# Kernel optimization log

Measured on AMD Instinct MI355X. Metric: run time of the kernel, lower is better.

## Reference

```python
import jax, jax.numpy as jnp
import numpy as np

BATCH, T, S, M = 512, 4096, 64, 125  # batch, seq_len, n_states, emission alphabet (5^3)


def setup_inputs() -> dict:
    key = jax.random.key(0)
    k1, k2, k3, k4 = jax.random.split(key, 4)
    obs = jax.random.randint(k1, (BATCH, T), 0, M)
    x = jax.nn.one_hot(obs, M, dtype=jnp.float32)            # [B, T, M] one-hot emissions
    I = jax.nn.softmax(jax.random.normal(k2, (1, S)))        # initial state distribution [1, S]
    A = jax.nn.softmax(jax.random.normal(k3, (S, S)), axis=-1)   # transition matrix, rows sum to 1
    Bm = jax.nn.softmax(jax.random.normal(k4, (M, S)), axis=0)   # emission matrix, cols sum to 1
    return {"x": x, "I": I, "A": A, "Bm": Bm}


def reference(x, I, A, Bm):
    """HMM forward algorithm with per-step normalization (default scaling branch of CgpHmmCell).

    Returns the accumulated log-likelihood [B, 1].
    """
    xT = jnp.swapaxes(x, 0, 1)  # [T, B, M] for scan over time

    # t = 1: R = I (broadcast over batch), old_loglik = 0
    E0 = xT[0] @ Bm                                  # [B, S]
    u0 = E0 * I                                      # unscaled alpha
    Z0 = jnp.sum(u0, axis=1, keepdims=True)          # [B, 1]
    carry0 = (u0 / Z0, jnp.log(Z0))

    def step(carry, x_t):
        alpha, ll = carry
        R = alpha @ A                                # [B, S] transition
        E = x_t @ Bm                                 # [B, S] emission lookup (one-hot matmul)
        u = E * R
        Z = jnp.sum(u, axis=1, keepdims=True)        # per-sequence scaling factor
        return (u / Z, ll + jnp.log(Z)), None

    (alpha, loglik), _ = jax.lax.scan(step, carry0, xT[1:])
    return loglik
```

## Files before the change

kernel.cpp:

```cpp
#include <hip/hip_runtime.h>


#define BATCH 512
#define T 4096
#define S 64
#define M 125
#define NPACK 22
#define WPB 4
#define BSTR 68
#define WSTR 17

typedef __attribute__((ext_vector_type(8))) short bf16x8;
typedef __attribute__((ext_vector_type(4))) float f32x4;

union BFU { unsigned u[4]; bf16x8 v; };

__device__ __forceinline__ unsigned pk_bf16(float a, float b) {
    unsigned ua = __float_as_uint(a) + 0x8000u;
    unsigned ub = __float_as_uint(b) + 0x8000u;
    return (ub & 0xFFFF0000u) | (ua >> 16);
}
__device__ __forceinline__ unsigned pk_bf16_rne(float a, float b) {
    unsigned ua = __float_as_uint(a); ua += 0x7FFFu + ((ua >> 16) & 1u);
    unsigned ub = __float_as_uint(b); ub += 0x7FFFu + ((ub >> 16) & 1u);
    return (ub & 0xFFFF0000u) | (ua >> 16);
}

__global__ __launch_bounds__(256) void extract_obs(const float4* __restrict__ x4,
                                                   unsigned char* __restrict__ obs) {
    const long long n4 = (long long)BATCH * T * M / 4;
    long long stride = (long long)gridDim.x * blockDim.x;
    for (long long i = (long long)blockIdx.x * blockDim.x + threadIdx.x; i < n4; i += stride) {
        float4 v = x4[i];
        if (v.x != 0.0f || v.y != 0.0f || v.z != 0.0f || v.w != 0.0f) {
            long long e = i * 4;
            if (v.x != 0.0f) { long long r = (e + 0) / M; obs[r] = (unsigned char)(e + 0 - r * M); }
            if (v.y != 0.0f) { long long r = (e + 1) / M; obs[r] = (unsigned char)(e + 1 - r * M); }
            if (v.z != 0.0f) { long long r = (e + 2) / M; obs[r] = (unsigned char)(e + 2 - r * M); }
            if (v.w != 0.0f) { long long r = (e + 3) / M; obs[r] = (unsigned char)(e + 3 - r * M); }
        }
    }
}

__global__ __launch_bounds__(256) void hmm_mfma(const unsigned char* __restrict__ obs,
                                                const float* __restrict__ Iv,
                                                const float* __restrict__ A,
                                                const float* __restrict__ Bm,
                                                float* __restrict__ out) {
    __shared__ __align__(16) float BmL[M * BSTR];
    __shared__ __align__(16) float ILds[S];
    __shared__ unsigned wscAll[WPB][32 * WSTR];

    const int tid = threadIdx.x, wv = tid >> 6, lane = tid & 63;
    const int s = lane & 15, g = lane >> 4;

    for (int i = tid; i < M * S; i += 256) BmL[(i >> 6) * BSTR + (i & 63)] = Bm[i];
    if (tid < S) ILds[tid] = Iv[tid];
    __syncthreads();

    BFU Af[4][2];
#pragma unroll
    for (int mt = 0; mt < 4; ++mt)
#pragma unroll
        for (int kf = 0; kf < 2; ++kf)
#pragma unroll
            for (int j2 = 0; j2 < 4; ++j2) {
                int k0 = kf * 32 + g * 8 + 2 * j2;
                float f0 = A[(size_t)k0 * S + mt * 16 + s];
                float f1 = A[(size_t)(k0 + 1) * S + mt * 16 + s];
                Af[mt][kf].u[j2] = pk_bf16_rne(f0, f1);
            }

    f32x4 I4[4];
#pragma unroll
    for (int mt = 0; mt < 4; ++mt) I4[mt] = *(const f32x4*)&ILds[mt * 16 + g * 4];

    const int W = blockIdx.x * WPB + wv;
    const int seq = W >> 1, hw = W & 1;
    const int chunk = hw * 16 + s;
    const bool c0wave = (hw == 0);
    const bool is_c0 = c0wave && (s == 0);

    const unsigned long long* orow = (const unsigned long long*)(obs + (size_t)seq * T);
    const int idx0 = chunk * 16 - 6;

    unsigned* wsc = wscAll[wv];

    BFU Bf[2];
#pragma unroll
    for (int kf = 0; kf < 2; ++kf)
#pragma unroll
        for (int j = 0; j < 4; ++j) Bf[kf].u[j] = 0x3F803F80u;

    float w[4][4];
    float Ls = 0.f, S0v = 0.f, c = 1.f;

    int i0 = idx0 < 0 ? 0 : idx0;
    unsigned long long u = orow[i0];

    for (int p = 0; p < NPACK; ++p) {
        int in_ = idx0 + p + 1;
        in_ = in_ < 0 ? 0 : (in_ > T / 8 - 1 ? T / 8 - 1 : in_);
        unsigned long long un = orow[in_];
        const bool ovp = c0wave && (p == 6);
#pragma unroll
        for (int k = 0; k < 8; ++k) {
            const int o = (int)((u >> (8 * k)) & 255ull);
            f32x4 E[4];
#pragma unroll
            for (int mt = 0; mt < 4; ++mt)
                E[mt] = *(const f32x4*)&BmL[o * BSTR + mt * 16 + g * 4];
            f32x4 acc[4];
#pragma unroll
            for (int mt = 0; mt < 4; ++mt) {
                f32x4 z = {0.f, 0.f, 0.f, 0.f};
                z = __builtin_amdgcn_mfma_f32_16x16x32_bf16(Af[mt][0].v, Bf[0].v, z, 0, 0, 0);
                acc[mt] = __builtin_amdgcn_mfma_f32_16x16x32_bf16(Af[mt][1].v, Bf[1].v, z, 0, 0, 0);
            }
#pragma unroll
            for (int mt = 0; mt < 4; ++mt)
#pragma unroll
                for (int r = 0; r < 4; ++r) {
                    float wv_ = acc[mt][r] * E[mt][r];
                    if (ovp && k == 0)
                        wv_ = is_c0 ? I4[mt][r] * E[mt][r] : wv_;
                    w[mt][r] = wv_;
                }
            float scale = 1.f;
            if (k == 7) {
                c = __uint_as_float(__builtin_amdgcn_ds_bpermute(s << 2, __float_as_uint(w[0][0])));
                c = fmaxf(c, 1e-37f);
                Ls += __log2f(c);
                scale = __builtin_amdgcn_rcpf(c);
            }
#pragma unroll
            for (int mt = 0; mt < 4; ++mt)
#pragma unroll
                for (int pr = 0; pr < 2; ++pr) {
                    float v0 = w[mt][2 * pr], v1 = w[mt][2 * pr + 1];
                    if (k == 7) { v0 *= scale; v1 *= scale; }
                    wsc[(2 * g + pr + 8 * mt) * WSTR + s] = pk_bf16(v0, v1);
                }
#pragma unroll
            for (int kf = 0; kf < 2; ++kf)
#pragma unroll
                for (int j = 0; j < 4; ++j)
                    Bf[kf].u[j] = wsc[(4 * g + j + 16 * kf) * WSTR + s];
        }
        if (p == 5) {
            float sw = 0.f;
#pragma unroll
            for (int mt = 0; mt < 4; ++mt)
#pragma unroll
                for (int r = 0; r < 4; ++r) sw += w[mt][r];
            sw += __shfl_xor(sw, 16);
            sw += __shfl_xor(sw, 32);
            S0v = (chunk == 0) ? Ls : (Ls + __log2f(sw) - __log2f(c));
        }
        u = un;
    }

    float sw = 0.f;
#pragma unroll
    for (int mt = 0; mt < 4; ++mt)
#pragma unroll
        for (int r = 0; r < 4; ++r) sw += w[mt][r];
    sw += __shfl_xor(sw, 16);
    sw += __shfl_xor(sw, 32);
    float Lfin = Ls + __log2f(sw) - __log2f(c) - S0v;
    if (lane < 16)
        atomicAdd(out + seq, Lfin * 0.6931471805599453f);
}

extern "C" void kernel_launch(void* const* d_in, const int* in_sizes, int n_in,
                              void* d_out, int out_size, void* d_ws, size_t ws_size,
                              hipStream_t stream) {
    const float* x  = (const float*)d_in[0];
    const float* I  = (const float*)d_in[1];
    const float* A  = (const float*)d_in[2];
    const float* Bm = (const float*)d_in[3];
    float* out = (float*)d_out;
    unsigned char* obs = (unsigned char*)d_ws;

    hipMemsetAsync(out, 0, (size_t)out_size * sizeof(float), stream);
    extract_obs<<<65536, 256, 0, stream>>>((const float4*)x, obs);
    hmm_mfma<<<256, WPB * 64, 0, stream>>>(obs, I, A, Bm, out);
}
```

Measured before the change: 1.347 ms.

## Split each sequence into more, shorter chunks with shorter burn-in

Each sequence is now split across 8 waves (128 chunks of 32 steps) instead of 2 waves (32 chunks of 128 steps), and the burn-in warm-up per chunk drops from 48 to 16 steps. Blocks grow to 8 waves and the grid grows to match. The aim is to shorten the serial recurrence each wave runs and raise parallelism, since the HMM kernel is latency-bound on its per-step chain. The trade-offs are a shorter warm-up, which may hurt convergence accuracy of the chunk boundaries, truncating instead of rounding bf16 packing, and an LDS padding change.

```diff
diff --git a/kernel.cpp b/kernel.cpp
--- a/kernel.cpp
+++ b/kernel.cpp
@@ -5,22 +5,22 @@
 #define T 4096
 #define S 64
 #define M 125
-#define NPACK 22
-#define WPB 4
+#define CHUNKP 4
+#define BURNP 2
+#define NPACK (CHUNKP + BURNP)
+#define WPB 8
 #define BSTR 68
-#define WSTR 17
+#define WSTR 20
 
 typedef __attribute__((ext_vector_type(8))) short bf16x8;
 typedef __attribute__((ext_vector_type(4))) float f32x4;
 
 union BFU { unsigned u[4]; bf16x8 v; };
 
-__device__ __forceinline__ unsigned pk_bf16(float a, float b) {
-    unsigned ua = __float_as_uint(a) + 0x8000u;
-    unsigned ub = __float_as_uint(b) + 0x8000u;
-    return (ub & 0xFFFF0000u) | (ua >> 16);
+__device__ __forceinline__ unsigned pk_trunc(float a, float b) {
+    return (__float_as_uint(b) & 0xFFFF0000u) | (__float_as_uint(a) >> 16);
 }
-__device__ __forceinline__ unsigned pk_bf16_rne(float a, float b) {
+__device__ __forceinline__ unsigned pk_rne(float a, float b) {
     unsigned ua = __float_as_uint(a); ua += 0x7FFFu + ((ua >> 16) & 1u);
     unsigned ub = __float_as_uint(b); ub += 0x7FFFu + ((ub >> 16) & 1u);
     return (ub & 0xFFFF0000u) | (ua >> 16);
@@ -42,11 +42,11 @@
     }
 }
 
-__global__ __launch_bounds__(256) void hmm_mfma(const unsigned char* __restrict__ obs,
-                                                const float* __restrict__ Iv,
-                                                const float* __restrict__ A,
-                                                const float* __restrict__ Bm,
-                                                float* __restrict__ out) {
+__global__ __launch_bounds__(512, 4) void hmm_mfma(const unsigned char* __restrict__ obs,
+                                                   const float* __restrict__ Iv,
+                                                   const float* __restrict__ A,
+                                                   const float* __restrict__ Bm,
+                                                   float* __restrict__ out) {
     __shared__ __align__(16) float BmL[M * BSTR];
     __shared__ __align__(16) float ILds[S];
     __shared__ unsigned wscAll[WPB][32 * WSTR];
@@ -54,7 +54,7 @@
     const int tid = threadIdx.x, wv = tid >> 6, lane = tid & 63;
     const int s = lane & 15, g = lane >> 4;
 
-    for (int i = tid; i < M * S; i += 256) BmL[(i >> 6) * BSTR + (i & 63)] = Bm[i];
+    for (int i = tid; i < M * S; i += WPB * 64) BmL[(i >> 6) * BSTR + (i & 63)] = Bm[i];
     if (tid < S) ILds[tid] = Iv[tid];
     __syncthreads();
 
@@ -66,23 +66,18 @@
 #pragma unroll
             for (int j2 = 0; j2 < 4; ++j2) {
                 int k0 = kf * 32 + g * 8 + 2 * j2;
-                float f0 = A[(size_t)k0 * S + mt * 16 + s];
-                float f1 = A[(size_t)(k0 + 1) * S + mt * 16 + s];
-                Af[mt][kf].u[j2] = pk_bf16_rne(f0, f1);
+                Af[mt][kf].u[j2] = pk_rne(A[(size_t)k0 * S + mt * 16 + s],
+                                          A[(size_t)(k0 + 1) * S + mt * 16 + s]);
             }
 
-    f32x4 I4[4];
-#pragma unroll
-    for (int mt = 0; mt < 4; ++mt) I4[mt] = *(const f32x4*)&ILds[mt * 16 + g * 4];
-
     const int W = blockIdx.x * WPB + wv;
-    const int seq = W >> 1, hw = W & 1;
+    const int seq = W >> 3, hw = W & 7;
     const int chunk = hw * 16 + s;
     const bool c0wave = (hw == 0);
     const bool is_c0 = c0wave && (s == 0);
 
     const unsigned long long* orow = (const unsigned long long*)(obs + (size_t)seq * T);
-    const int idx0 = chunk * 16 - 6;
+    const int idx0 = chunk * CHUNKP - BURNP;
 
     unsigned* wsc = wscAll[wv];
 
@@ -102,7 +97,7 @@
         int in_ = idx0 + p + 1;
         in_ = in_ < 0 ? 0 : (in_ > T / 8 - 1 ? T / 8 - 1 : in_);
         unsigned long long un = orow[in_];
-        const bool ovp = c0wave && (p == 6);
+        const bool ovp = c0wave && (p == BURNP);
 #pragma unroll
         for (int k = 0; k < 8; ++k) {
             const int o = (int)((u >> (8 * k)) & 255ull);
@@ -123,7 +118,7 @@
                 for (int r = 0; r < 4; ++r) {
                     float wv_ = acc[mt][r] * E[mt][r];
                     if (ovp && k == 0)
-                        wv_ = is_c0 ? I4[mt][r] * E[mt][r] : wv_;
+                        wv_ = is_c0 ? ILds[mt * 16 + g * 4 + r] * E[mt][r] : wv_;
                     w[mt][r] = wv_;
                 }
             float scale = 1.f;
@@ -139,7 +134,7 @@
                 for (int pr = 0; pr < 2; ++pr) {
                     float v0 = w[mt][2 * pr], v1 = w[mt][2 * pr + 1];
                     if (k == 7) { v0 *= scale; v1 *= scale; }
-                    wsc[(2 * g + pr + 8 * mt) * WSTR + s] = pk_bf16(v0, v1);
+                    wsc[(2 * g + pr + 8 * mt) * WSTR + s] = pk_trunc(v0, v1);
                 }
 #pragma unroll
             for (int kf = 0; kf < 2; ++kf)
@@ -147,7 +142,7 @@
                 for (int j = 0; j < 4; ++j)
                     Bf[kf].u[j] = wsc[(4 * g + j + 16 * kf) * WSTR + s];
         }
-        if (p == 5) {
+        if (p == BURNP - 1) {
             float sw = 0.f;
 #pragma unroll
             for (int mt = 0; mt < 4; ++mt)
@@ -184,5 +179,5 @@
 
     hipMemsetAsync(out, 0, (size_t)out_size * sizeof(float), stream);
     extract_obs<<<65536, 256, 0, stream>>>((const float4*)x, obs);
-    hmm_mfma<<<256, WPB * 64, 0, stream>>>(obs, I, A, Bm, out);
+    hmm_mfma<<<(BATCH * 8) / WPB, WPB * 64, 0, stream>>>(obs, I, A, Bm, out);
 }
```

Result: no change. 1.367 ms (+1.5%).
